# Performance work log

Measured on AMD Instinct MI355X. Metric: run time of the kernel, lower is better.

The kernel has to match this reference:

```python
import jax, jax.numpy as jnp
import numpy as np

K = 3
TAPS = K ** 3  # 27 taps of the 3x3x3 kernel


def _conv3d(x, w, b):
    # x: (B,C,T,H,W), w: (O,I,kT,kH,kW), stride 1, pad 1
    y = jax.lax.conv_general_dilated(
        x, w, window_strides=(1, 1, 1),
        padding=((1, 1), (1, 1), (1, 1)),
        dimension_numbers=('NCDHW', 'OIDHW', 'NCDHW'))
    return y + b[None, :, None, None, None]


def _bilinear(xt, ph, pw):
    # xt: (B,C,T,H,W) temporally-shifted features; ph/pw: (B,T,H,W) float coords
    # zero padding outside the spatial extent (matches deform-conv semantics)
    B, C, T, H, W = xt.shape
    h0 = jnp.floor(ph)
    w0 = jnp.floor(pw)
    lh = (ph - h0)[:, None]  # (B,1,T,H,W)
    lw = (pw - w0)[:, None]
    h0i = h0.astype(jnp.int32)
    w0i = w0.astype(jnp.int32)
    xf = xt.reshape(B, C, T, H * W)

    def gather(hi, wi):
        valid = (hi >= 0) & (hi < H) & (wi >= 0) & (wi < W)
        idx = (jnp.clip(hi, 0, H - 1) * W + jnp.clip(wi, 0, W - 1)).reshape(B, 1, T, H * W)
        v = jnp.take_along_axis(xf, jnp.broadcast_to(idx, (B, C, T, H * W)), axis=3)
        return v.reshape(B, C, T, H, W) * valid[:, None].astype(xt.dtype)

    v00 = gather(h0i, w0i)
    v01 = gather(h0i, w0i + 1)
    v10 = gather(h0i + 1, w0i)
    v11 = gather(h0i + 1, w0i + 1)
    return (v00 * (1 - lh) * (1 - lw) + v01 * (1 - lh) * lw
            + v10 * lh * (1 - lw) + v11 * lh * lw)


def _dcn_hw(x, w_off, b_off, w, b):
    # DeformConvPack_d with dimension='HW': offsets deform H/W only, temporal taps rigid
    B, C, T, H, W = x.shape
    off = _conv3d(x, w_off, b_off).reshape(B, TAPS, 2, T, H, W)  # (dy, dx) per tap
    x_pad = jnp.pad(x, ((0, 0), (0, 0), (1, 1), (0, 0), (0, 0)))  # zero pad T
    hh = jnp.arange(H, dtype=x.dtype)[None, None, :, None]
    ww = jnp.arange(W, dtype=x.dtype)[None, None, None, :]
    out = jnp.zeros((B, w.shape[0], T, H, W), x.dtype)
    k = 0
    for kt in range(K):
        xt = x_pad[:, :, kt:kt + T]  # rigid temporal shift for this tap
        for kh in range(K):
            for kw in range(K):
                ph = hh + (kh - 1) + off[:, k, 0]
                pw = ww + (kw - 1) + off[:, k, 1]
                s = _bilinear(xt, ph, pw)  # (B,C,T,H,W)
                out = out + jnp.einsum('bcthw,oc->bothw', s, w[:, :, kt, kh, kw])
                k += 1
    return out + b[None, :, None, None, None]


def setup_inputs() -> dict:
    key = jax.random.key(0)
    ks = jax.random.split(key, 9)
    nf, B, T, H, W = 64, 1, 7, 96, 96
    sc = 1.0 / np.sqrt(nf * TAPS)
    return {
        'x': jax.random.normal(ks[0], (B, nf, T, H, W), jnp.float32),
        'w_off0': jax.random.normal(ks[1], (2 * TAPS, nf, K, K, K), jnp.float32) * 0.01,
        'b_off0': jax.random.normal(ks[2], (2 * TAPS,), jnp.float32) * 0.01,
        'w0': jax.random.normal(ks[3], (nf, nf, K, K, K), jnp.float32) * sc,
        'b0': jax.random.normal(ks[4], (nf,), jnp.float32) * 0.01,
        'w_off1': jax.random.normal(ks[5], (2 * TAPS, nf, K, K, K), jnp.float32) * 0.01,
        'b_off1': jax.random.normal(ks[6], (2 * TAPS,), jnp.float32) * 0.01,
        'w1': jax.random.normal(ks[7], (nf, nf, K, K, K), jnp.float32) * sc,
        'b1': jax.random.normal(ks[8], (nf,), jnp.float32) * 0.01,
    }


def reference(x, w_off0, b_off0, w0, b0, w_off1, b_off1, w1, b1):
    y = _dcn_hw(x, w_off0, b_off0, w0, b0)
    y = jnp.where(y > 0, y, 0.1 * y)  # LeakyReLU(0.1)
    return _dcn_hw(y, w_off1, b_off1, w1, b1) + x
```

## Files before the change

### kernel.cpp

```cpp
#include <hip/hip_runtime.h>
#include <hip/hip_fp16.h>

#define T_DIM 7
#define H_DIM 96
#define W_DIM 96
#define HW    (H_DIM*W_DIM)
#define L_DIM (T_DIM*HW)
#define NTAPS 27

#define TR 8
#define TC 16
#define HR (TR+8)
#define HC (TC+8)
#define HROWB (HC*128)
#define HALO_B (HR*HROWB)
#define WBUF_OFF HALO_B
#define SOFF_OFF (HALO_B + 16384)
#define SOFF_STRIDE 108
#define SMEM_B (SOFF_OFF + 128*SOFF_STRIDE)

typedef __attribute__((ext_vector_type(8))) _Float16 f16x8;
typedef __attribute__((ext_vector_type(4))) float f32x4;

#define GLOAD16(gp, lp) \
    __builtin_amdgcn_global_load_lds((const __attribute__((address_space(1))) unsigned int*)(gp), \
                                     (__attribute__((address_space(3))) unsigned int*)(lp), 16, 0, 0)

__global__ void zfill(int4* __restrict__ z)
{
    z[threadIdx.x] = make_int4(0, 0, 0, 0);
}

__global__ void prep_weights(const float* __restrict__ woff0,
                             const float* __restrict__ w0,
                             const float* __restrict__ woff1,
                             const float* __restrict__ w1,
                             unsigned short* __restrict__ dst)
{
    int idx = blockIdx.x * 256 + threadIdx.x;
    const int per = NTAPS * 64 * 64;
    if (idx >= 4 * per) return;
    int which = idx / per;
    int r     = idx % per;
    int tap   = r / 4096;
    int o     = (r >> 6) & 63;
    int c     = r & 63;
    const float* src = (which == 0) ? woff0 : (which == 1) ? w0
                     : (which == 2) ? woff1 : w1;
    int omax = (which == 0 || which == 2) ? 54 : 64;
    float v = 0.f;
    if (o < omax) v = src[(o * 64 + c) * NTAPS + tap];
    __half h = __float2half(v);
    int slot = (((c >> 3) + o) & 7);
    int pos  = tap * 4096 + o * 64 + slot * 8 + (c & 7);
    dst[which * per + pos] = __half_as_ushort(h);
}

__global__ void transpose_x(const float* __restrict__ x, unsigned* __restrict__ xt2)
{
    __shared__ float tile[64][65];
    const int tid = threadIdx.x;
    const int lb  = blockIdx.x * 64;
    const int ln  = tid & 63;
    const int q   = tid >> 6;
#pragma unroll
    for (int i = 0; i < 16; ++i) {
        int c = q + 4 * i;
        tile[ln][c] = x[(size_t)c * L_DIM + lb + ln];
    }
    __syncthreads();
    const int ln2 = tid & 31, q2 = tid >> 5;
#pragma unroll
    for (int i = 0; i < 8; ++i) {
        int ll = q2 + 8 * i;
        __half2 h2 = __float22half2_rn(make_float2(tile[ll][2*ln2], tile[ll][2*ln2+1]));
        xt2[(size_t)(lb + ll) * 32 + ln2] = *reinterpret_cast<unsigned*>(&h2);
    }
}

#define STAGE_SLAB(KT) { \
    int tp_ = t + (KT) - 1; \
    bool tvz_ = (tp_ >= 0) && (tp_ < T_DIM); \
    const unsigned char* sb_ = xb + (size_t)(tvz_ ? tp_ : 0) * HW * 128; \
    _Pragma("unroll") \
    for (int i = 0; i < 12; ++i) { \
        int p16_ = tid + i * 256; \
        int hr_ = p16_ / 192; \
        int rem_ = p16_ - hr_ * 192; \
        int hc_ = rem_ >> 3; \
        int sl_ = rem_ & 7; \
        int ch_ = (sl_ - hc_) & 7; \
        int gr_ = row0 - 4 + hr_; \
        int gc_ = col0 - 4 + hc_; \
        bool ok_ = tvz_ && (gr_ >= 0) && (gr_ < H_DIM) && (gc_ >= 0) && (gc_ < W_DIM); \
        const unsigned char* src_ = ok_ \
            ? (sb_ + (size_t)(gr_ * W_DIM + gc_) * 128 + ch_ * 16) \
            : (zb + sl_ * 16); \
        GLOAD16(src_, smem + (i << 12) + (wv << 10)); \
    } }

#define WSTAGE(WG, K) { \
    const unsigned char* ws_ = (WG) + (size_t)(K) * 8192 + tid * 16; \
    unsigned char* ld_ = smem + WBUF_OFF + (((K) & 1) << 13) + (wv << 10); \
    GLOAD16(ws_,        ld_); \
    GLOAD16(ws_ + 4096, ld_ + 4096); }

#define READ_OFF(MT, K) ({ \
    unsigned u_ = *(const unsigned*)(smem + SOFF_OFF + \
        ((2 * wv + (MT)) * 16 + lr) * SOFF_STRIDE + (K) * 4); \
    __half22float2(*reinterpret_cast<__half2*>(&u_)); })

#define GATHER_D(MT, O2, A0, A1) { \
    float ph_ = (float)(row0 + 2 * wv + (MT) + kh - 1) + (O2).x; \
    float pw_ = (float)(col0 + lr + kw - 1) + (O2).y; \
    float hf_ = floorf(ph_), wf_ = floorf(pw_); \
    float lh_ = ph_ - hf_, lw_ = pw_ - wf_; \
    int sr_ = min(max((int)hf_ - row0 + 4, 0), HR - 2); \
    int sc_ = min(max((int)wf_ - col0 + 4, 0), HC - 2); \
    __half2 cw00_ = __float2half2_rn((1.f - lh_) * (1.f - lw_)); \
    __half2 cw01_ = __float2half2_rn((1.f - lh_) * lw_); \
    __half2 cw10_ = __float2half2_rn(lh_ * (1.f - lw_)); \
    __half2 cw11_ = __float2half2_rn(lh_ * lw_); \
    const unsigned char* r0_ = smem + sr_ * HROWB; \
    const unsigned char* r1_ = r0_ + HROWB; \
    int c0a_ = sc_ * 128 + (((lk + sc_) & 7) << 4); \
    int c0b_ = sc_ * 128 + (((lk + 4 + sc_) & 7) << 4); \
    int c1a_ = (sc_ + 1) * 128 + (((lk + 1 + sc_) & 7) << 4); \
    int c1b_ = (sc_ + 1) * 128 + (((lk + 5 + sc_) & 7) << 4); \
    f16x8 v00a_ = *(const f16x8*)(r0_ + c0a_), v00b_ = *(const f16x8*)(r0_ + c0b_); \
    f16x8 v01a_ = *(const f16x8*)(r0_ + c1a_), v01b_ = *(const f16x8*)(r0_ + c1b_); \
    f16x8 v10a_ = *(const f16x8*)(r1_ + c0a_), v10b_ = *(const f16x8*)(r1_ + c0b_); \
    f16x8 v11a_ = *(const f16x8*)(r1_ + c1a_), v11b_ = *(const f16x8*)(r1_ + c1b_); \
    __align__(16) __half2 va_[8]; \
    const __half2* p00a_ = (const __half2*)&v00a_; \
    const __half2* p01a_ = (const __half2*)&v01a_; \
    const __half2* p10a_ = (const __half2*)&v10a_; \
    const __half2* p11a_ = (const __half2*)&v11a_; \
    const __half2* p00b_ = (const __half2*)&v00b_; \
    const __half2* p01b_ = (const __half2*)&v01b_; \
    const __half2* p10b_ = (const __half2*)&v10b_; \
    const __half2* p11b_ = (const __half2*)&v11b_; \
    _Pragma("unroll") \
    for (int d = 0; d < 4; ++d) { \
        __half2 s0_ = __hmul2(p00a_[d], cw00_); \
        s0_ = __hfma2(p01a_[d], cw01_, s0_); \
        s0_ = __hfma2(p10a_[d], cw10_, s0_); \
        s0_ = __hfma2(p11a_[d], cw11_, s0_); \
        va_[d] = s0_; \
        __half2 s1_ = __hmul2(p00b_[d], cw00_); \
        s1_ = __hfma2(p01b_[d], cw01_, s1_); \
        s1_ = __hfma2(p10b_[d], cw10_, s1_); \
        s1_ = __hfma2(p11b_[d], cw11_, s1_); \
        va_[4 + d] = s1_; \
    } \
    A0 = *reinterpret_cast<f16x8*>(&va_[0]); \
    A1 = *reinterpret_cast<f16x8*>(&va_[4]); }

#define GATHER_C(MT, A0, A1) { \
    int sr_ = 2 * wv + (MT) + kh + 3, sc_ = lr + kw + 3; \
    const unsigned char* cell_ = smem + sr_ * HROWB + sc_ * 128; \
    int4 z0_ = *(const int4*)(cell_ + (((lk + sc_) & 7) << 4)); \
    int4 z1_ = *(const int4*)(cell_ + (((lk + 4 + sc_) & 7) << 4)); \
    A0 = *reinterpret_cast<f16x8*>(&z0_); \
    A1 = *reinterpret_cast<f16x8*>(&z1_); }

#define MFMA_F16(A, B, C) __builtin_amdgcn_mfma_f32_16x16x32_f16( \
    A, *reinterpret_cast<f16x8*>(&(B)), C, 0, 0, 0)

#define RUN_PHASE(DEF, WGBLP) { \
    const unsigned char* wgbl_ = (WGBLP); \
    asm volatile("s_waitcnt lgkmcnt(0)" ::: "memory"); \
    __builtin_amdgcn_s_barrier(); \
    STAGE_SLAB(0); \
    WSTAGE(wgbl_, 0); \
    float2 oc0, oc1, on0, on1; \
    oc0 = make_float2(0.f, 0.f); oc1 = oc0; on0 = oc0; on1 = oc0; \
    if (DEF) { oc0 = READ_OFF(0, 0); oc1 = READ_OFF(1, 0); } \
    asm volatile("s_waitcnt vmcnt(0)" ::: "memory"); \
    __builtin_amdgcn_s_barrier(); \
    __builtin_amdgcn_sched_barrier(0); \
    _Pragma("unroll 1") \
    for (int kt = 0; kt < 3; ++kt) { \
        if (kt > 0) { \
            asm volatile("s_waitcnt lgkmcnt(0)" ::: "memory"); \
            __builtin_amdgcn_s_barrier(); \
            STAGE_SLAB(kt); \
            asm volatile("s_waitcnt vmcnt(0)" ::: "memory"); \
            __builtin_amdgcn_s_barrier(); \
            __builtin_amdgcn_sched_barrier(0); \
        } \
        _Pragma("unroll 1") \
        for (int k9 = 0; k9 < 9; ++k9) { \
            int k = kt * 9 + k9; \
            if (k > 0) { \
                asm volatile("s_waitcnt vmcnt(0) lgkmcnt(0)" ::: "memory"); \
                __builtin_amdgcn_s_barrier(); \
                __builtin_amdgcn_sched_barrier(0); \
            } \
            if (k + 1 < NTAPS) { \
                WSTAGE(wgbl_, k + 1); \
                if (DEF) { on0 = READ_OFF(0, k + 1); on1 = READ_OFF(1, k + 1); } \
            } \
            int kh = k9 / 3, kw = k9 - (k9 / 3) * 3; \
            f16x8 a00, a01, a10, a11; \
            if (DEF) { GATHER_D(0, oc0, a00, a01); GATHER_D(1, oc1, a10, a11); } \
            else     { GATHER_C(0, a00, a01);      GATHER_C(1, a10, a11); } \
            const unsigned char* br_ = smem + WBUF_OFF + ((k & 1) << 13) + lr * 128; \
            _Pragma("unroll") \
            for (int n = 0; n < 4; ++n) { \
                f16x8 b0_ = *(const f16x8*)(br_ + n * 2048 + s0); \
                f16x8 b1_ = *(const f16x8*)(br_ + n * 2048 + s1); \
                acc[0][n] = MFMA_F16(a00, b0_, acc[0][n]); \
                acc[0][n] = MFMA_F16(a01, b1_, acc[0][n]); \
                acc[1][n] = MFMA_F16(a10, b0_, acc[1][n]); \
                acc[1][n] = MFMA_F16(a11, b1_, acc[1][n]); \
            } \
            oc0 = on0; oc1 = on1; \
        } \
    } }

template<int EPI>
__global__ __launch_bounds__(256, 2)
void dcn_zp(const unsigned short* __restrict__ xin,
            const unsigned short* __restrict__ Wtoff,
            const unsigned short* __restrict__ Wtm,
            const float* __restrict__ boff,
            const float* __restrict__ bmain,
            const float* __restrict__ resid,
            const unsigned char* __restrict__ zb,
            float* __restrict__ outf,
            unsigned short* __restrict__ outh)
{
    __shared__ __align__(16) unsigned char smem[SMEM_B];

    const int tid  = threadIdx.x;
    const int wv   = tid >> 6, lane = tid & 63;
    const int lr   = lane & 15, lk = lane >> 4;

    const int bid = blockIdx.x;
    const int wg  = (bid & 7) * 63 + (bid >> 3);
    const int t   = wg / 72;
    const int rg  = (wg % 72) / 6;
    const int cg  = wg % 6;
    const int row0 = rg * TR;
    const int col0 = cg * TC;

    const unsigned char* xb = (const unsigned char*)xin;

    const int s0 = ((lk + lr) & 7) << 4;
    const int s1 = ((lk + 4 + lr) & 7) << 4;

    f32x4 acc[2][4];
#pragma unroll
    for (int mt = 0; mt < 2; ++mt)
#pragma unroll
        for (int n = 0; n < 4; ++n) acc[mt][n] = (f32x4){0.f, 0.f, 0.f, 0.f};

    RUN_PHASE(false, (const unsigned char*)Wtoff);

#pragma unroll
    for (int n = 0; n < 4; ++n) {
        int o = n * 16 + lr;
        if (o < 54) {
            float bvA = boff[o];
#pragma unroll
            for (int mt = 0; mt < 2; ++mt)
#pragma unroll
                for (int i = 0; i < 4; ++i) {
                    int l = (2 * wv + mt) * 16 + lk * 4 + i;
                    float vv = acc[mt][n][i] + bvA;
                    *(unsigned short*)(smem + SOFF_OFF + l * SOFF_STRIDE + o * 2) =
                        __half_as_ushort(__float2half(vv));
                }
        }
    }
    __syncthreads();

#pragma unroll
    for (int mt = 0; mt < 2; ++mt)
#pragma unroll
        for (int n = 0; n < 4; ++n) acc[mt][n] = (f32x4){0.f, 0.f, 0.f, 0.f};

    RUN_PHASE(true, (const unsigned char*)Wtm);

    float bv[4];
#pragma unroll
    for (int n = 0; n < 4; ++n) bv[n] = bmain[n * 16 + lr];

    if (EPI == 1) {
#pragma unroll
        for (int mt = 0; mt < 2; ++mt) {
            size_t lrowmt = (size_t)t * HW + (size_t)(row0 + 2 * wv + mt) * W_DIM + col0;
#pragma unroll
            for (int n = 0; n < 4; ++n)
#pragma unroll
                for (int i = 0; i < 4; ++i) {
                    int lc = lk * 4 + i;
                    float vv = acc[mt][n][i] + bv[n];
                    vv = (vv > 0.f) ? vv : 0.1f * vv;
                    outh[(lrowmt + lc) * 64 + n * 16 + lr] =
                        __half_as_ushort(__float2half(vv));
                }
        }
    } else {
        __syncthreads();
        float* tf = (float*)(smem + (wv << 13));
#pragma unroll
        for (int mt = 0; mt < 2; ++mt)
#pragma unroll
            for (int n = 0; n < 4; ++n)
#pragma unroll
                for (int i = 0; i < 4; ++i) {
                    int l = mt * 16 + lk * 4 + i;
                    int och = n * 16 + lr;
                    tf[l * 64 + ((och + 2 * l) & 63)] = acc[mt][n][i] + bv[n];
                }
        asm volatile("s_waitcnt lgkmcnt(0)" ::: "memory");
        __builtin_amdgcn_sched_barrier(0);
        int j = lane & 15, gq = lane >> 4;
#pragma unroll
        for (int mt = 0; mt < 2; ++mt) {
            size_t lrowmt = (size_t)t * HW + (size_t)(row0 + 2 * wv + mt) * W_DIM + col0;
#pragma unroll
            for (int it = 0; it < 16; ++it) {
                int och = gq * 16 + it;
                int l = mt * 16 + j;
                float val = tf[l * 64 + ((och + 2 * l) & 63)];
                size_t gi = (size_t)och * L_DIM + lrowmt + j;
                outf[gi] = val + resid[gi];
            }
        }
    }
}

extern "C" void kernel_launch(void* const* d_in, const int* in_sizes, int n_in,
                              void* d_out, int out_size, void* d_ws, size_t ws_size,
                              hipStream_t stream)
{
    const float* x     = (const float*)d_in[0];
    const float* woff0 = (const float*)d_in[1];
    const float* boff0 = (const float*)d_in[2];
    const float* w0    = (const float*)d_in[3];
    const float* b0    = (const float*)d_in[4];
    const float* woff1 = (const float*)d_in[5];
    const float* boff1 = (const float*)d_in[6];
    const float* w1    = (const float*)d_in[7];
    const float* b1    = (const float*)d_in[8];
    float* out = (float*)d_out;

    unsigned char* ws = (unsigned char*)d_ws;
    unsigned short* Wt  = (unsigned short*)ws;
    unsigned short* xt  = (unsigned short*)(ws + 884736);
    unsigned short* y   = (unsigned short*)(ws + 9142272);
    unsigned char*  zb  = ws + 17399808;

    zfill<<<1, 256, 0, stream>>>((int4*)zb);
    prep_weights<<<1728, 256, 0, stream>>>(woff0, w0, woff1, w1, Wt);
    transpose_x<<<1008, 256, 0, stream>>>(x, (unsigned*)xt);

    const int grid = T_DIM * (H_DIM / TR) * (W_DIM / TC);
    const int WSZ  = NTAPS * 64 * 64;

    dcn_zp<1><<<grid, 256, 0, stream>>>(xt, Wt,           Wt + WSZ,     boff0, b0, nullptr, zb, nullptr, y);
    dcn_zp<2><<<grid, 256, 0, stream>>>(y,  Wt + 2 * WSZ, Wt + 3 * WSZ, boff1, b1, x,       zb, out, nullptr);
}
```

Before: 128.6 us.

## Load MFMA weight fragments directly from global into registers, drop per-tap barriers

After: 225.9 us. +75.7%, slower.

```diff
diff --git a/kernel.cpp b/kernel.cpp
--- a/kernel.cpp
+++ b/kernel.cpp
@@ -14,8 +14,7 @@
 #define HC (TC+8)
 #define HROWB (HC*128)
 #define HALO_B (HR*HROWB)
-#define WBUF_OFF HALO_B
-#define SOFF_OFF (HALO_B + 16384)
+#define SOFF_OFF HALO_B
 #define SOFF_STRIDE 108
 #define SMEM_B (SOFF_OFF + 128*SOFF_STRIDE)
 
@@ -51,9 +50,7 @@
     float v = 0.f;
     if (o < omax) v = src[(o * 64 + c) * NTAPS + tap];
     __half h = __float2half(v);
-    int slot = (((c >> 3) + o) & 7);
-    int pos  = tap * 4096 + o * 64 + slot * 8 + (c & 7);
-    dst[which * per + pos] = __half_as_ushort(h);
+    dst[which * per + tap * 4096 + o * 64 + c] = __half_as_ushort(h);
 }
 
 __global__ void transpose_x(const float* __restrict__ x, unsigned* __restrict__ xt2)
@@ -99,11 +96,12 @@
         GLOAD16(src_, smem + (i << 12) + (wv << 10)); \
     } }
 
-#define WSTAGE(WG, K) { \
-    const unsigned char* ws_ = (WG) + (size_t)(K) * 8192 + tid * 16; \
-    unsigned char* ld_ = smem + WBUF_OFF + (((K) & 1) << 13) + (wv << 10); \
-    GLOAD16(ws_,        ld_); \
-    GLOAD16(ws_ + 4096, ld_ + 4096); }
+#define BLOAD(WG, K, BR) { \
+    const unsigned char* bp_ = (WG) + (size_t)(K) * 8192 + lr * 128 + lk * 16; \
+    BR[0] = *(const int4*)(bp_);          BR[1] = *(const int4*)(bp_ + 64); \
+    BR[2] = *(const int4*)(bp_ + 2048);   BR[3] = *(const int4*)(bp_ + 2048 + 64); \
+    BR[4] = *(const int4*)(bp_ + 4096);   BR[5] = *(const int4*)(bp_ + 4096 + 64); \
+    BR[6] = *(const int4*)(bp_ + 6144);   BR[7] = *(const int4*)(bp_ + 6144 + 64); }
 
 #define READ_OFF(MT, K) ({ \
     unsigned u_ = *(const unsigned*)(smem + SOFF_OFF + \
@@ -172,7 +170,8 @@
     asm volatile("s_waitcnt lgkmcnt(0)" ::: "memory"); \
     __builtin_amdgcn_s_barrier(); \
     STAGE_SLAB(0); \
-    WSTAGE(wgbl_, 0); \
+    int4 bc[8], bn[8]; \
+    BLOAD(wgbl_, 0, bc); \
     float2 oc0, oc1, on0, on1; \
     oc0 = make_float2(0.f, 0.f); oc1 = oc0; on0 = oc0; on1 = oc0; \
     if (DEF) { oc0 = READ_OFF(0, 0); oc1 = READ_OFF(1, 0); } \
@@ -192,44 +191,40 @@
         _Pragma("unroll 1") \
         for (int k9 = 0; k9 < 9; ++k9) { \
             int k = kt * 9 + k9; \
-            if (k > 0) { \
-                asm volatile("s_waitcnt vmcnt(0) lgkmcnt(0)" ::: "memory"); \
-                __builtin_amdgcn_s_barrier(); \
-                __builtin_amdgcn_sched_barrier(0); \
-            } \
             if (k + 1 < NTAPS) { \
-                WSTAGE(wgbl_, k + 1); \
+                BLOAD(wgbl_, k + 1, bn); \
                 if (DEF) { on0 = READ_OFF(0, k + 1); on1 = READ_OFF(1, k + 1); } \
             } \
             int kh = k9 / 3, kw = k9 - (k9 / 3) * 3; \
             f16x8 a00, a01, a10, a11; \
             if (DEF) { GATHER_D(0, oc0, a00, a01); GATHER_D(1, oc1, a10, a11); } \
             else     { GATHER_C(0, a00, a01);      GATHER_C(1, a10, a11); } \
-            const unsigned char* br_ = smem + WBUF_OFF + ((k & 1) << 13) + lr * 128; \
             _Pragma("unroll") \
             for (int n = 0; n < 4; ++n) { \
-                f16x8 b0_ = *(const f16x8*)(br_ + n * 2048 + s0); \
-                f16x8 b1_ = *(const f16x8*)(br_ + n * 2048 + s1); \
-                acc[0][n] = MFMA_F16(a00, b0_, acc[0][n]); \
-                acc[0][n] = MFMA_F16(a01, b1_, acc[0][n]); \
-                acc[1][n] = MFMA_F16(a10, b0_, acc[1][n]); \
-                acc[1][n] = MFMA_F16(a11, b1_, acc[1][n]); \
+                acc[0][n] = MFMA_F16(a00, bc[2*n],     acc[0][n]); \
+                acc[0][n] = MFMA_F16(a01, bc[2*n + 1], acc[0][n]); \
+                acc[1][n] = MFMA_F16(a10, bc[2*n],     acc[1][n]); \
+                acc[1][n] = MFMA_F16(a11, bc[2*n + 1], acc[1][n]); \
             } \
-            oc0 = on0; oc1 = on1; \
+            if (k + 1 < NTAPS) { \
+                _Pragma("unroll") \
+                for (int q8 = 0; q8 < 8; ++q8) bc[q8] = bn[q8]; \
+                oc0 = on0; oc1 = on1; \
+            } \
         } \
     } }
 
 template<int EPI>
 __global__ __launch_bounds__(256, 2)
-void dcn_zp(const unsigned short* __restrict__ xin,
-            const unsigned short* __restrict__ Wtoff,
-            const unsigned short* __restrict__ Wtm,
-            const float* __restrict__ boff,
-            const float* __restrict__ bmain,
-            const float* __restrict__ resid,
-            const unsigned char* __restrict__ zb,
-            float* __restrict__ outf,
-            unsigned short* __restrict__ outh)
+void dcn_bl1(const unsigned short* __restrict__ xin,
+             const unsigned short* __restrict__ Wtoff,
+             const unsigned short* __restrict__ Wtm,
+             const float* __restrict__ boff,
+             const float* __restrict__ bmain,
+             const float* __restrict__ resid,
+             const unsigned char* __restrict__ zb,
+             float* __restrict__ outf,
+             unsigned short* __restrict__ outh)
 {
     __shared__ __align__(16) unsigned char smem[SMEM_B];
 
@@ -246,9 +241,6 @@
     const int col0 = cg * TC;
 
     const unsigned char* xb = (const unsigned char*)xin;
-
-    const int s0 = ((lk + lr) & 7) << 4;
-    const int s1 = ((lk + 4 + lr) & 7) << 4;
 
     f32x4 acc[2][4];
 #pragma unroll
@@ -361,6 +353,6 @@
     const int grid = T_DIM * (H_DIM / TR) * (W_DIM / TC);
     const int WSZ  = NTAPS * 64 * 64;
 
-    dcn_zp<1><<<grid, 256, 0, stream>>>(xt, Wt,           Wt + WSZ,     boff0, b0, nullptr, zb, nullptr, y);
-    dcn_zp<2><<<grid, 256, 0, stream>>>(y,  Wt + 2 * WSZ, Wt + 3 * WSZ, boff1, b1, x,       zb, out, nullptr);
-}
+    dcn_bl1<1><<<grid, 256, 0, stream>>>(xt, Wt,           Wt + WSZ,     boff0, b0, nullptr, zb, nullptr, y);
+    dcn_bl1<2><<<grid, 256, 0, stream>>>(y,  Wt + 2 * WSZ, Wt + 3 * WSZ, boff1, b1, x,       zb, out, nullptr);
+}
```

## Enlarge spatial tile to 12 rows with 6 waves, spill offsets to global

Applied to the files above, without the earlier changes.

Measured after the change: 237.7 us. 1.85x slower.

```diff
diff --git a/kernel.cpp b/kernel.cpp
--- a/kernel.cpp
+++ b/kernel.cpp
@@ -8,16 +8,14 @@
 #define L_DIM (T_DIM*HW)
 #define NTAPS 27
 
-#define TR 8
+#define TR 12
 #define TC 16
 #define HR (TR+8)
 #define HC (TC+8)
 #define HROWB (HC*128)
 #define HALO_B (HR*HROWB)
 #define WBUF_OFF HALO_B
-#define SOFF_OFF (HALO_B + 16384)
-#define SOFF_STRIDE 108
-#define SMEM_B (SOFF_OFF + 128*SOFF_STRIDE)
+#define SMEM_B (WBUF_OFF + 16384)
 
 typedef __attribute__((ext_vector_type(8))) _Float16 f16x8;
 typedef __attribute__((ext_vector_type(4))) float f32x4;
@@ -83,8 +81,8 @@
     bool tvz_ = (tp_ >= 0) && (tp_ < T_DIM); \
     const unsigned char* sb_ = xb + (size_t)(tvz_ ? tp_ : 0) * HW * 128; \
     _Pragma("unroll") \
-    for (int i = 0; i < 12; ++i) { \
-        int p16_ = tid + i * 256; \
+    for (int i = 0; i < 10; ++i) { \
+        int p16_ = tid + i * 384; \
         int hr_ = p16_ / 192; \
         int rem_ = p16_ - hr_ * 192; \
         int hc_ = rem_ >> 3; \
@@ -96,18 +94,19 @@
         const unsigned char* src_ = ok_ \
             ? (sb_ + (size_t)(gr_ * W_DIM + gc_) * 128 + ch_ * 16) \
             : (zb + sl_ * 16); \
-        GLOAD16(src_, smem + (i << 12) + (wv << 10)); \
+        GLOAD16(src_, smem + i * 6144 + (wv << 10)); \
     } }
 
 #define WSTAGE(WG, K) { \
-    const unsigned char* ws_ = (WG) + (size_t)(K) * 8192 + tid * 16; \
-    unsigned char* ld_ = smem + WBUF_OFF + (((K) & 1) << 13) + (wv << 10); \
-    GLOAD16(ws_,        ld_); \
-    GLOAD16(ws_ + 4096, ld_ + 4096); }
+    if (wv < 4) { \
+        const unsigned char* ws_ = (WG) + (size_t)(K) * 8192 + tid * 16; \
+        unsigned char* ld_ = smem + WBUF_OFF + (((K) & 1) << 13) + (wv << 10); \
+        GLOAD16(ws_,        ld_); \
+        GLOAD16(ws_ + 4096, ld_ + 4096); \
+    } }
 
 #define READ_OFF(MT, K) ({ \
-    unsigned u_ = *(const unsigned*)(smem + SOFF_OFF + \
-        ((2 * wv + (MT)) * 16 + lr) * SOFF_STRIDE + (K) * 4); \
+    unsigned u_ = offg[(size_t)(lrow0 + (MT) * W_DIM + lr) * 32 + (K)]; \
     __half22float2(*reinterpret_cast<__half2*>(&u_)); })
 
 #define GATHER_D(MT, O2, A0, A1) { \
@@ -220,16 +219,17 @@
     } }
 
 template<int EPI>
-__global__ __launch_bounds__(256, 2)
-void dcn_zp(const unsigned short* __restrict__ xin,
-            const unsigned short* __restrict__ Wtoff,
-            const unsigned short* __restrict__ Wtm,
-            const float* __restrict__ boff,
-            const float* __restrict__ bmain,
-            const float* __restrict__ resid,
-            const unsigned char* __restrict__ zb,
-            float* __restrict__ outf,
-            unsigned short* __restrict__ outh)
+__global__ __launch_bounds__(384, 2)
+void dcn_g12(const unsigned short* __restrict__ xin,
+             const unsigned short* __restrict__ Wtoff,
+             const unsigned short* __restrict__ Wtm,
+             const float* __restrict__ boff,
+             const float* __restrict__ bmain,
+             const float* __restrict__ resid,
+             const unsigned char* __restrict__ zb,
+             unsigned* __restrict__ offg,
+             float* __restrict__ outf,
+             unsigned short* __restrict__ outh)
 {
     __shared__ __align__(16) unsigned char smem[SMEM_B];
 
@@ -238,12 +238,13 @@
     const int lr   = lane & 15, lk = lane >> 4;
 
     const int bid = blockIdx.x;
-    const int wg  = (bid & 7) * 63 + (bid >> 3);
-    const int t   = wg / 72;
-    const int rg  = (wg % 72) / 6;
+    const int wg  = (bid & 7) * 42 + (bid >> 3);
+    const int t   = wg / 48;
+    const int rg  = (wg % 48) / 6;
     const int cg  = wg % 6;
     const int row0 = rg * TR;
     const int col0 = cg * TC;
+    const int lrow0 = t * HW + (row0 + 2 * wv) * W_DIM + col0;
 
     const unsigned char* xb = (const unsigned char*)xin;
 
@@ -258,20 +259,22 @@
 
     RUN_PHASE(false, (const unsigned char*)Wtoff);
 
-#pragma unroll
-    for (int n = 0; n < 4; ++n) {
-        int o = n * 16 + lr;
-        if (o < 54) {
-            float bvA = boff[o];
-#pragma unroll
-            for (int mt = 0; mt < 2; ++mt)
-#pragma unroll
-                for (int i = 0; i < 4; ++i) {
-                    int l = (2 * wv + mt) * 16 + lk * 4 + i;
-                    float vv = acc[mt][n][i] + bvA;
-                    *(unsigned short*)(smem + SOFF_OFF + l * SOFF_STRIDE + o * 2) =
-                        __half_as_ushort(__float2half(vv));
-                }
+    {
+        unsigned short* og16 = (unsigned short*)offg;
+#pragma unroll
+        for (int n = 0; n < 4; ++n) {
+            int o = n * 16 + lr;
+            if (o < 54) {
+                float bvA = boff[o];
+#pragma unroll
+                for (int mt = 0; mt < 2; ++mt)
+#pragma unroll
+                    for (int i = 0; i < 4; ++i) {
+                        size_t absloc = (size_t)lrow0 + mt * W_DIM + lk * 4 + i;
+                        float vv = acc[mt][n][i] + bvA;
+                        og16[absloc * 64 + o] = __half_as_ushort(__float2half(vv));
+                    }
+            }
         }
     }
     __syncthreads();
@@ -290,7 +293,7 @@
     if (EPI == 1) {
 #pragma unroll
         for (int mt = 0; mt < 2; ++mt) {
-            size_t lrowmt = (size_t)t * HW + (size_t)(row0 + 2 * wv + mt) * W_DIM + col0;
+            size_t lrowmt = (size_t)lrow0 + mt * W_DIM;
 #pragma unroll
             for (int n = 0; n < 4; ++n)
 #pragma unroll
@@ -320,7 +323,7 @@
         int j = lane & 15, gq = lane >> 4;
 #pragma unroll
         for (int mt = 0; mt < 2; ++mt) {
-            size_t lrowmt = (size_t)t * HW + (size_t)(row0 + 2 * wv + mt) * W_DIM + col0;
+            size_t lrowmt = (size_t)lrow0 + mt * W_DIM;
 #pragma unroll
             for (int it = 0; it < 16; ++it) {
                 int och = gq * 16 + it;
@@ -352,7 +355,8 @@
     unsigned short* Wt  = (unsigned short*)ws;
     unsigned short* xt  = (unsigned short*)(ws + 884736);
     unsigned short* y   = (unsigned short*)(ws + 9142272);
-    unsigned char*  zb  = ws + 17399808;
+    unsigned*       offg= (unsigned*)(ws + 17399808);
+    unsigned char*  zb  = ws + 25657344;
 
     zfill<<<1, 256, 0, stream>>>((int4*)zb);
     prep_weights<<<1728, 256, 0, stream>>>(woff0, w0, woff1, w1, Wt);
@@ -361,6 +365,6 @@
     const int grid = T_DIM * (H_DIM / TR) * (W_DIM / TC);
     const int WSZ  = NTAPS * 64 * 64;
 
-    dcn_zp<1><<<grid, 256, 0, stream>>>(xt, Wt,           Wt + WSZ,     boff0, b0, nullptr, zb, nullptr, y);
-    dcn_zp<2><<<grid, 256, 0, stream>>>(y,  Wt + 2 * WSZ, Wt + 3 * WSZ, boff1, b1, x,       zb, out, nullptr);
-}
+    dcn_g12<1><<<grid, 384, 0, stream>>>(xt, Wt,           Wt + WSZ,     boff0, b0, nullptr, zb, offg, nullptr, y);
+    dcn_g12<2><<<grid, 384, 0, stream>>>(y,  Wt + 2 * WSZ, Wt + 3 * WSZ, boff1, b1, x,       zb, offg, out, nullptr);
+}
```
